# Performance work log

Hardware: AMD Instinct MI355X
Metric: run time of the kernel (lower is better)

## Reference

```python
import jax, jax.numpy as jnp
import numpy as np

D_MODEL = 512
N_HEADS = 8
MAX_DEPTH = 4
D_FF = 4 * D_MODEL
B, L = 4, 2048


def setup_inputs() -> dict:
    key = jax.random.key(0)
    ks = jax.random.split(key, 16)
    s = 0.02
    inp = {
        "x": jax.random.normal(ks[0], (B, L, D_MODEL), dtype=jnp.float32),
        # attention pre-norm
        "ln1_g": jnp.ones((D_MODEL,), jnp.float32),
        "ln1_b": jnp.zeros((D_MODEL,), jnp.float32),
        # MultiheadAttention in_proj (3D, D) and out_proj (D, D), torch (out, in) layout
        "Wqkv": jax.random.normal(ks[1], (3 * D_MODEL, D_MODEL), jnp.float32) * s,
        "bqkv": jnp.zeros((3 * D_MODEL,), jnp.float32),
        "Wo": jax.random.normal(ks[2], (D_MODEL, D_MODEL), jnp.float32) * s,
        "bo": jnp.zeros((D_MODEL,), jnp.float32),
        # FFN pre-norm + MLP
        "ln2_g": jnp.ones((D_MODEL,), jnp.float32),
        "ln2_b": jnp.zeros((D_MODEL,), jnp.float32),
        "W1": jax.random.normal(ks[3], (D_FF, D_MODEL), jnp.float32) * s,
        "b1": jnp.zeros((D_FF,), jnp.float32),
        "W2": jax.random.normal(ks[4], (D_MODEL, D_FF), jnp.float32) * s,
        "b2": jnp.zeros((D_MODEL,), jnp.float32),
        # token-choice depth router: LayerNorm + Linear(D,D) + GELU + Linear(D,max_depth)
        "rn_g": jnp.ones((D_MODEL,), jnp.float32),
        "rn_b": jnp.zeros((D_MODEL,), jnp.float32),
        "Rw1": jax.random.normal(ks[5], (D_MODEL, D_MODEL), jnp.float32) * s,
        "Rb1": jnp.zeros((D_MODEL,), jnp.float32),
        "Rw2": jax.random.normal(ks[6], (MAX_DEPTH, D_MODEL), jnp.float32) * s,
        "Rb2": jnp.zeros((MAX_DEPTH,), jnp.float32),
    }
    return inp


def _layernorm(x, g, b, eps=1e-5):
    mu = jnp.mean(x, axis=-1, keepdims=True)
    var = jnp.var(x, axis=-1, keepdims=True)
    return (x - mu) * jax.lax.rsqrt(var + eps) * g + b


def _block(x, ln1_g, ln1_b, Wqkv, bqkv, Wo, bo, ln2_g, ln2_b, W1, b1, W2, b2):
    Bb, Ll, D = x.shape
    H = N_HEADS
    dh = D // H
    # pre-norm self-attention
    h = _layernorm(x, ln1_g, ln1_b)
    qkv = h @ Wqkv.T + bqkv                      # (B, L, 3D)
    q, k, v = jnp.split(qkv, 3, axis=-1)
    q = q.reshape(Bb, Ll, H, dh)
    k = k.reshape(Bb, Ll, H, dh)
    v = v.reshape(Bb, Ll, H, dh)
    scores = jnp.einsum("blhd,bmhd->bhlm", q, k) / jnp.sqrt(jnp.float32(dh))
    attn = jax.nn.softmax(scores, axis=-1)
    o = jnp.einsum("bhlm,bmhd->blhd", attn, v).reshape(Bb, Ll, D)
    x = x + (o @ Wo.T + bo)
    # pre-norm FFN (exact-erf GELU, matching torch nn.GELU default)
    h2 = _layernorm(x, ln2_g, ln2_b)
    f = jax.nn.gelu(h2 @ W1.T + b1, approximate=False) @ W2.T + b2
    return x + f


def reference(x, ln1_g, ln1_b, Wqkv, bqkv, Wo, bo, ln2_g, ln2_b, W1, b1, W2, b2,
              rn_g, rn_b, Rw1, Rb1, Rw2, Rb2):
    # --- token-choice depth router (eval mode: argmax) ---
    rh = _layernorm(x, rn_g, rn_b)
    rh = jax.nn.gelu(rh @ Rw1.T + Rb1, approximate=False)
    router_logits = rh @ Rw2.T + Rb2             # (B, L, MAX_DEPTH)
    depths = jnp.argmax(router_logits, axis=-1) + 1  # (B, L) in [1, MAX_DEPTH]
    # --- dense recursion with torch.where-style selection ---
    cur = x
    for level in range(1, MAX_DEPTH + 1):
        upd = _block(cur, ln1_g, ln1_b, Wqkv, bqkv, Wo, bo,
                     ln2_g, ln2_b, W1, b1, W2, b2)
        keep = (depths >= level)[..., None]      # (B, L, 1)
        cur = jnp.where(keep, upd, cur)
    return cur, depths, router_logits
```

## Files before the change

kernel.cpp:

```cpp
#include <hip/hip_runtime.h>

typedef unsigned short u16;
typedef __attribute__((ext_vector_type(8))) short short8;
typedef __attribute__((ext_vector_type(4))) short s16x4;
typedef __attribute__((ext_vector_type(4))) float floatx4;
typedef __attribute__((ext_vector_type(4))) unsigned short u16x4;

#define NTOK 8192
#define DMODEL 512
#define DFF 2048
#define LSEQ 2048
#define RMARGIN 1e-3f

__device__ __forceinline__ u16 f2bf(float f) {
    union { float f; unsigned u; } x; x.f = f;
    unsigned r = (x.u + 0x7fffu + ((x.u >> 16) & 1u)) >> 16;
    return (u16)r;
}
__device__ __forceinline__ float bf2f(u16 h) {
    union { unsigned u; float f; } x; x.u = ((unsigned)h) << 16;
    return x.f;
}

__device__ __forceinline__ float geluf(float x) {
    return 0.5f * x * (1.0f + erff(x * 0.70710678118654752f));
}

__device__ __forceinline__ void gload_lds16(const void* g, void* l) {
    __builtin_amdgcn_global_load_lds(
        (const __attribute__((address_space(1))) void*)g,
        (__attribute__((address_space(3))) void*)l,
        16, 0, 0);
}

__device__ __forceinline__ s16x4 pack_p(float p0, float p1, float p2, float p3) {
    union { float f; unsigned u; } a{p0}, b{p1}, c{p2}, d{p3};
    union { unsigned u[2]; s16x4 s; } r;
    r.u[0] = (a.u >> 16) | (b.u & 0xffff0000u);
    r.u[1] = (c.u >> 16) | (d.u & 0xffff0000u);
    return r.s;
}

__global__ __launch_bounds__(256) void cvt_w(const float* __restrict__ wq,
                                             const float* __restrict__ wo,
                                             const float* __restrict__ w1,
                                             const float* __restrict__ w2,
                                             u16* __restrict__ out) {
    int i = blockIdx.x * 256 + threadIdx.x;
    float v;
    if (i < 786432)       v = wq[i];
    else if (i < 1048576) v = wo[i - 786432];
    else if (i < 2097152) v = w1[i - 1048576];
    else                  v = w2[i - 2097152];
    out[i] = f2bf(v);
}

__global__ __launch_bounds__(256) void copy_f32(const float* __restrict__ a,
                                                float* __restrict__ b) {
    size_t i = ((size_t)blockIdx.x * 256 + threadIdx.x) * 4;
    *(floatx4*)&b[i] = *(const floatx4*)&a[i];
}

__global__ __launch_bounds__(256) void cvt_rw1(const float* __restrict__ Rw1,
                                               u16* __restrict__ out) {
    const int i = blockIdx.x * 256 + threadIdx.x;
    const int n = i >> 9, k = i & 511;
    const float v = Rw1[i];
    const u16 hi = f2bf(v);
    const u16 lo = f2bf(v - bf2f(hi));
    out[(size_t)n * 1536 + k] = hi;
    out[(size_t)n * 1536 + 512 + k] = hi;
    out[(size_t)n * 1536 + 1024 + k] = lo;
}

__global__ __launch_bounds__(256) void cvt_split(const float* __restrict__ x,
                                                 u16* __restrict__ out,
                                                 int* __restrict__ cnt) {
    if (blockIdx.x == 0 && threadIdx.x == 0) *cnt = 0;
    const int i = blockIdx.x * 256 + threadIdx.x;
    const int base = i * 4;
    const int row = base >> 9, k = base & 511;
    const floatx4 v = *(const floatx4*)&x[base];
    u16x4 h, l;
#pragma unroll
    for (int e = 0; e < 4; ++e) {
        h[e] = f2bf(v[e]);
        l[e] = f2bf(v[e] - bf2f(h[e]));
    }
    u16* o = out + (size_t)row * 1536;
    *(u16x4*)&o[k] = h;
    *(u16x4*)&o[512 + k] = l;
    *(u16x4*)&o[1024 + k] = h;
}

template<bool OUTF32>
__global__ __launch_bounds__(256)
void ln_k(const float* __restrict__ x, const float* __restrict__ g,
          const float* __restrict__ bb, void* __restrict__ outp) {
    const int row = blockIdx.x * 4 + (threadIdx.x >> 6);
    const int lane = threadIdx.x & 63;
    const float* xr = x + (size_t)row * DMODEL;
    const int c0 = lane * 4, c1 = c0 + 256;
    floatx4 a = *(const floatx4*)&xr[c0];
    floatx4 b = *(const floatx4*)&xr[c1];
    float s = 0.f, sq = 0.f;
#pragma unroll
    for (int e = 0; e < 4; ++e) { s += a[e]; sq += a[e] * a[e]; }
#pragma unroll
    for (int e = 0; e < 4; ++e) { s += b[e]; sq += b[e] * b[e]; }
#pragma unroll
    for (int m = 32; m >= 1; m >>= 1) {
        s += __shfl_xor(s, m);
        sq += __shfl_xor(sq, m);
    }
    const float mean = s * (1.f / 512.f);
    const float rstd = rsqrtf(sq * (1.f / 512.f) - mean * mean + 1e-5f);
    floatx4 g0 = *(const floatx4*)&g[c0];
    floatx4 g1 = *(const floatx4*)&g[c1];
    floatx4 b0 = *(const floatx4*)&bb[c0];
    floatx4 b1 = *(const floatx4*)&bb[c1];
    floatx4 y0, y1;
#pragma unroll
    for (int e = 0; e < 4; ++e) {
        y0[e] = (a[e] - mean) * rstd * g0[e] + b0[e];
        y1[e] = (b[e] - mean) * rstd * g1[e] + b1[e];
    }
    if (OUTF32) {
        float* o = (float*)outp + (size_t)row * DMODEL;
        *(floatx4*)&o[c0] = y0;
        *(floatx4*)&o[c1] = y1;
    } else {
        u16* o = (u16*)outp + (size_t)row * DMODEL;
        u16x4 p0, p1;
#pragma unroll
        for (int e = 0; e < 4; ++e) { p0[e] = f2bf(y0[e]); p1[e] = f2bf(y1[e]); }
        *(u16x4*)&o[c0] = p0;
        *(u16x4*)&o[c1] = p1;
    }
}

template<int EPI, int BN>
__global__ __launch_bounds__(256, 2)
void gemm_bt(const u16* __restrict__ A, const u16* __restrict__ Bw,
             const float* __restrict__ bias,
             u16* __restrict__ Cb, float* __restrict__ Cf,
             const float* __restrict__ res, const float* __restrict__ depth,
             u16* __restrict__ Cv,
             float aux, int N, int K) {
    constexpr int NJ = BN / 32;
    __shared__ __align__(16) u16 As[128 * 32];
    __shared__ __align__(16) u16 Bs[BN * 32];
    const int tid = threadIdx.x;
    const int lane = tid & 63;
    const int w = tid >> 6;
    const int wm = (w >> 1) * 64;
    const int wn = (w & 1) * (BN / 2);
    const int mBase = blockIdx.x * 128;
    const int nBase = blockIdx.y * BN;
    const int q4 = lane >> 4, rl = lane & 15;

    floatx4 acc[4][NJ];
#pragma unroll
    for (int i = 0; i < 4; ++i)
#pragma unroll
        for (int j = 0; j < NJ; ++j) acc[i][j] = (floatx4){0.f, 0.f, 0.f, 0.f};

    const int i0 = tid, i1 = tid + 256;
    const int ar0 = i0 >> 2, ac0 = ((i0 & 3) ^ ((i0 >> 3) & 3)) * 8;
    const int ar1 = i1 >> 2, ac1 = ((i1 & 3) ^ ((i1 >> 3) & 3)) * 8;
    const u16* pA0 = A + (size_t)(mBase + ar0) * K + ac0;
    const u16* pA1 = A + (size_t)(mBase + ar1) * K + ac1;
    const u16* pB0 = Bw + (size_t)(nBase + ar0) * K + ac0;
    const u16* pB1 = (BN == 128) ? Bw + (size_t)(nBase + ar1) * K + ac1 : pB0;
    u16* lA0 = &As[i0 * 8];
    u16* lA1 = &As[i1 * 8];
    u16* lB0 = &Bs[i0 * 8];
    u16* lB1 = (BN == 128) ? &Bs[i1 * 8] : lB0;

    for (int k0 = 0; k0 < K; k0 += 32) {
        gload_lds16(pA0, lA0);
        gload_lds16(pA1, lA1);
        gload_lds16(pB0, lB0);
        if (BN == 128) gload_lds16(pB1, lB1);
        pA0 += 32; pA1 += 32; pB0 += 32;
        if (BN == 128) pB1 += 32;
        __syncthreads();
        short8 af[4], bf[NJ];
#pragma unroll
        for (int t = 0; t < 4; ++t) {
            const int r = wm + t * 16 + rl;
            af[t] = *(const short8*)&As[r * 32 + (q4 ^ ((r >> 1) & 3)) * 8];
        }
#pragma unroll
        for (int t = 0; t < NJ; ++t) {
            const int r = wn + t * 16 + rl;
            bf[t] = *(const short8*)&Bs[r * 32 + (q4 ^ ((r >> 1) & 3)) * 8];
        }
#pragma unroll
        for (int ti = 0; ti < 4; ++ti)
#pragma unroll
            for (int tj = 0; tj < NJ; ++tj)
                acc[ti][tj] = __builtin_amdgcn_mfma_f32_16x16x32_bf16(
                    af[ti], bf[tj], acc[ti][tj], 0, 0, 0);
        __syncthreads();
    }

#pragma unroll
    for (int ti = 0; ti < 4; ++ti) {
        const int r0 = mBase + wm + ti * 16 + q4 * 4;
#pragma unroll
        for (int tj = 0; tj < NJ; ++tj) {
            const int c = nBase + wn + tj * 16 + rl;
            const float bv = bias[c];
            if (EPI == 0) {
                if (nBase < 1024) {
                    const float sc = (nBase < 512) ? aux : 1.0f;
#pragma unroll
                    for (int rr = 0; rr < 4; ++rr)
                        Cb[(size_t)(r0 + rr) * 1024 + c] =
                            f2bf((acc[ti][tj][rr] + bv) * sc);
                } else {
                    const int cm = c - 1024;
                    const int hh = cm >> 6, dh = cm & 63;
                    const int bb2 = r0 >> 11, kv = r0 & 2047;
                    u16x4 pk;
#pragma unroll
                    for (int rr = 0; rr < 4; ++rr)
                        pk[rr] = f2bf(acc[ti][tj][rr] + bv);
                    *(u16x4*)&Cv[((size_t)(bb2 * 8 + hh) * 64 + dh) * 2048 + kv] = pk;
                }
            } else {
#pragma unroll
                for (int rr = 0; rr < 4; ++rr) {
                    const int r = r0 + rr;
                    const float v = acc[ti][tj][rr] + bv;
                    if (EPI == 1) {
                        Cb[(size_t)r * N + c] = f2bf(geluf(v));
                    } else if (EPI == 2) {
                        Cf[(size_t)r * N + c] = res[(size_t)r * N + c] + v;
                    } else if (EPI == 3) {
                        if (depth[r] >= aux)
                            Cf[(size_t)r * N + c] = res[(size_t)r * N + c] + v;
                    } else {
                        Cf[(size_t)r * N + c] = geluf(v);
                    }
                }
            }
        }
    }
}

__global__ __launch_bounds__(256, 2)
void attn_k(const u16* __restrict__ qk, const u16* __restrict__ vT,
            u16* __restrict__ o) {
    const int qt = blockIdx.x;
    const int bh = blockIdx.y;
    const int b = bh >> 3, h = bh & 7;
    const int tid = threadIdx.x, lane = tid & 63, w = tid >> 6;
    const int tok0 = b * LSEQ;
    const int qrow0 = qt * 128 + w * 32;
    const int q4 = lane >> 4, rl = lane & 15;

    __shared__ __align__(16) u16 Kt[128 * 64];
    __shared__ __align__(16) u16 Vt[64 * 128];

    const u16* vbase = vT + (size_t)bh * 64 * 2048;

    short8 qf[2][2];
#pragma unroll
    for (int nt = 0; nt < 2; ++nt)
#pragma unroll
        for (int ks = 0; ks < 2; ++ks)
            qf[nt][ks] = *(const short8*)&qk[(size_t)(tok0 + qrow0 + nt * 16 + rl) * 1024
                                             + h * 64 + ks * 32 + q4 * 8];

    floatx4 oacc[4][2];
#pragma unroll
    for (int dt = 0; dt < 4; ++dt)
#pragma unroll
        for (int nt = 0; nt < 2; ++nt) oacc[dt][nt] = (floatx4){0.f, 0.f, 0.f, 0.f};
    float lsum[2] = {0.f, 0.f};

    const u16* kp0 = &Kt[rl * 64 + ((q4 ^ (rl & 7))) * 8];
    const u16* kp1 = &Kt[rl * 64 + (((4 + q4) ^ (rl & 7))) * 8];

    for (int kt = 0; kt < 16; ++kt) {
        const int kv0 = kt * 128;
        __syncthreads();
#pragma unroll
        for (int it = 0; it < 4; ++it) {
            const int i = it * 256 + tid;
            const int r = i >> 3;
            const int c = ((i & 7) ^ (r & 7)) * 8;
            gload_lds16(&qk[(size_t)(tok0 + kv0 + r) * 1024 + 512 + h * 64 + c],
                        &Kt[i * 8]);
        }
#pragma unroll
        for (int it = 0; it < 4; ++it) {
            const int i = it * 256 + tid;
            const int dh = i >> 4;
            const int ch = (i & 15) ^ (dh & 15);
            gload_lds16(&vbase[(size_t)dh * 2048 + kv0 + ch * 8], &Vt[i * 8]);
        }
        __syncthreads();

#pragma unroll
        for (int mt = 0; mt < 8; ++mt) {
            const short8 kf0 = *(const short8*)&kp0[mt * 1024];
            const short8 kf1 = *(const short8*)&kp1[mt * 1024];
            floatx4 s[2];
#pragma unroll
            for (int nt = 0; nt < 2; ++nt) {
                s[nt] = __builtin_amdgcn_mfma_f32_16x16x32_bf16(kf0, qf[nt][0],
                        (floatx4){0.f, 0.f, 0.f, 0.f}, 0, 0, 0);
                s[nt] = __builtin_amdgcn_mfma_f32_16x16x32_bf16(kf1, qf[nt][1],
                        s[nt], 0, 0, 0);
            }
            s16x4 pb[2];
#pragma unroll
            for (int nt = 0; nt < 2; ++nt) {
                const float p0 = exp2f(s[nt][0]);
                const float p1 = exp2f(s[nt][1]);
                const float p2 = exp2f(s[nt][2]);
                const float p3 = exp2f(s[nt][3]);
                lsum[nt] += (p0 + p1) + (p2 + p3);
                pb[nt] = pack_p(p0, p1, p2, p3);
            }
            const int ct = 2 * mt + (q4 >> 1);
            const u16* vp = &Vt[(ct ^ rl) * 8 + (q4 & 1) * 4 + rl * 128];
#pragma unroll
            for (int dt = 0; dt < 4; ++dt) {
                const s16x4 vf = *(const s16x4*)&vp[dt * 2048];
#pragma unroll
                for (int nt = 0; nt < 2; ++nt)
                    oacc[dt][nt] = __builtin_amdgcn_mfma_f32_16x16x16bf16_1k(
                        vf, pb[nt], oacc[dt][nt], 0, 0, 0);
            }
        }
    }

#pragma unroll
    for (int nt = 0; nt < 2; ++nt) {
        float l = lsum[nt];
        l += __shfl_xor(l, 16);
        l += __shfl_xor(l, 32);
        const float inv = 1.0f / l;
        const size_t row = tok0 + qrow0 + nt * 16 + rl;
#pragma unroll
        for (int dt = 0; dt < 4; ++dt) {
            u16x4 pk;
#pragma unroll
            for (int rr = 0; rr < 4; ++rr) pk[rr] = f2bf(oacc[dt][nt][rr] * inv);
            *(u16x4*)&o[row * DMODEL + h * 64 + dt * 16 + q4 * 4] = pk;
        }
    }
}

__global__ __launch_bounds__(256)
void router_logits_f32(const float* __restrict__ rr, const float* __restrict__ Rw2,
                       const float* __restrict__ Rb2, float* __restrict__ logits,
                       float* __restrict__ depthf, int* __restrict__ cnt,
                       int* __restrict__ list) {
    const int t = blockIdx.x * 4 + (threadIdx.x >> 6);
    const int lane = threadIdx.x & 63;
    const float* xr = rr + (size_t)t * 512;
    const int c0 = lane * 4, c1 = c0 + 256;
    floatx4 a = *(const floatx4*)&xr[c0];
    floatx4 b = *(const floatx4*)&xr[c1];
    float s[4];
#pragma unroll
    for (int d = 0; d < 4; ++d) {
        const float* wr = Rw2 + d * 512;
        floatx4 wa = *(const floatx4*)&wr[c0];
        floatx4 wb = *(const floatx4*)&wr[c1];
        float acc = 0.f;
#pragma unroll
        for (int e = 0; e < 4; ++e) acc += a[e] * wa[e];
#pragma unroll
        for (int e = 0; e < 4; ++e) acc += b[e] * wb[e];
        s[d] = acc;
    }
#pragma unroll
    for (int m = 32; m >= 1; m >>= 1)
#pragma unroll
        for (int d = 0; d < 4; ++d) s[d] += __shfl_xor(s[d], m);
    if (lane == 0) {
        float v[4];
        float bv = -1e30f; int best = 0;
#pragma unroll
        for (int d = 0; d < 4; ++d) {
            v[d] = s[d] + Rb2[d];
            logits[(size_t)t * 4 + d] = v[d];
            if (v[d] > bv) { bv = v[d]; best = d; }
        }
        float second = -1e30f;
#pragma unroll
        for (int d = 0; d < 4; ++d)
            if (d != best) second = fmaxf(second, v[d]);
        depthf[t] = (float)(best + 1);
        if (bv - second < RMARGIN) {
            int idx = atomicAdd(cnt, 1);
            list[idx] = t;
        }
    }
}

__global__ __launch_bounds__(256)
void router_exact(const float* __restrict__ rh, const float* __restrict__ Rw1,
                  const float* __restrict__ Rb1, const float* __restrict__ Rw2,
                  const float* __restrict__ Rb2, const int* __restrict__ cnt,
                  const int* __restrict__ list, float* __restrict__ logits,
                  float* __restrict__ depthf) {
    __shared__ float rhs[512];
    __shared__ double rrd[512];
    __shared__ double lg[4];
    const int n = *cnt;
    const int tid = threadIdx.x;
    for (int ii = blockIdx.x; ii < n; ii += gridDim.x) {
        const int t = list[ii];
        rhs[tid] = rh[(size_t)t * 512 + tid];
        rhs[tid + 256] = rh[(size_t)t * 512 + 256 + tid];
        __syncthreads();
#pragma unroll
        for (int oo = 0; oo < 2; ++oo) {
            const int nn = tid + oo * 256;
            double acc = (double)Rb1[nn];
            const float* wrow = Rw1 + (size_t)nn * 512;
            for (int k = 0; k < 512; ++k)
                acc = fma((double)rhs[k], (double)wrow[k], acc);
            rrd[nn] = 0.5 * acc * (1.0 + erf(acc * 0.70710678118654752440));
        }
        __syncthreads();
        const int w = tid >> 6, lane = tid & 63;
        double acc2 = 0.0;
        for (int k = lane; k < 512; k += 64)
            acc2 += rrd[k] * (double)Rw2[w * 512 + k];
#pragma unroll
        for (int m = 32; m >= 1; m >>= 1) acc2 += __shfl_xor(acc2, m);
        if (lane == 0) lg[w] = acc2 + (double)Rb2[w];
        __syncthreads();
        if (tid == 0) {
            double bv = -1e300; int best = 0;
#pragma unroll
            for (int d = 0; d < 4; ++d) {
                const double v = lg[d];
                logits[(size_t)t * 4 + d] = (float)v;
                if (v > bv) { bv = v; best = d; }
            }
            depthf[t] = (float)(best + 1);
        }
        __syncthreads();
    }
}

extern "C" void kernel_launch(void* const* d_in, const int* in_sizes, int n_in,
                              void* d_out, int out_size, void* d_ws, size_t ws_size,
                              hipStream_t stream) {
    (void)in_sizes; (void)n_in; (void)out_size; (void)ws_size;
    const float* x    = (const float*)d_in[0];
    const float* ln1g = (const float*)d_in[1];
    const float* ln1b = (const float*)d_in[2];
    const float* Wqkv = (const float*)d_in[3];
    const float* bqkv = (const float*)d_in[4];
    const float* Wo   = (const float*)d_in[5];
    const float* bo   = (const float*)d_in[6];
    const float* ln2g = (const float*)d_in[7];
    const float* ln2b = (const float*)d_in[8];
    const float* W1   = (const float*)d_in[9];
    const float* b1   = (const float*)d_in[10];
    const float* W2   = (const float*)d_in[11];
    const float* b2   = (const float*)d_in[12];
    const float* rng  = (const float*)d_in[13];
    const float* rnb  = (const float*)d_in[14];
    const float* Rw1  = (const float*)d_in[15];
    const float* Rb1  = (const float*)d_in[16];
    const float* Rw2  = (const float*)d_in[17];
    const float* Rb2  = (const float*)d_in[18];

    float* cur    = (float*)d_out;
    float* depthf = cur + (size_t)NTOK * DMODEL;
    float* logits = depthf + NTOK;

    char* ws = (char*)d_ws;
    float* xmid = (float*)ws;
    u16* sbuf   = (u16*)(ws + 16777216);
    u16* qk     = (u16*)(ws + 25165824);
    u16* ffb    = (u16*)(ws + 41943040);
    u16* vTb    = (u16*)(ws + 75497472);
    u16* wbf    = (u16*)(ws + 83886080);

    u16* rw1s   = (u16*)(ws + 16777216);
    int* rcnt   = (int*)(ws + 18874368);
    int* rlist  = rcnt + 16;
    u16* asplit = ffb;
    float* rrf  = (float*)qk;

    u16* wq = wbf;
    u16* wo = wbf + 786432;
    u16* w1 = wbf + 1048576;
    u16* w2 = wbf + 2097152;

    const float qsc = 0.125f * 1.4426950408889634f;

    cvt_w<<<12288, 256, 0, stream>>>(Wqkv, Wo, W1, W2, wbf);
    copy_f32<<<4096, 256, 0, stream>>>(x, cur);

    ln_k<true><<<2048, 256, 0, stream>>>(x, rng, rnb, xmid);
    cvt_rw1<<<1024, 256, 0, stream>>>(Rw1, rw1s);
    cvt_split<<<4096, 256, 0, stream>>>(xmid, asplit, rcnt);
    gemm_bt<4, 64><<<dim3(64, 8), 256, 0, stream>>>(
        asplit, rw1s, Rb1, nullptr, rrf, nullptr, nullptr, nullptr, 0.f, 512, 1536);
    router_logits_f32<<<2048, 256, 0, stream>>>(rrf, Rw2, Rb2, logits, depthf,
                                                rcnt, rlist);
    router_exact<<<128, 256, 0, stream>>>(xmid, Rw1, Rb1, Rw2, Rb2, rcnt, rlist,
                                          logits, depthf);

    for (int level = 1; level <= 4; ++level) {
        ln_k<false><<<2048, 256, 0, stream>>>(cur, ln1g, ln1b, sbuf);
        gemm_bt<0, 128><<<dim3(64, 12), 256, 0, stream>>>(
            sbuf, wq, bqkv, qk, nullptr, nullptr, nullptr, vTb, qsc, 1536, 512);
        attn_k<<<dim3(16, 32), 256, 0, stream>>>(qk, vTb, sbuf);
        gemm_bt<2, 64><<<dim3(64, 8), 256, 0, stream>>>(
            sbuf, wo, bo, nullptr, xmid, cur, nullptr, nullptr, 0.f, 512, 512);
        ln_k<false><<<2048, 256, 0, stream>>>(xmid, ln2g, ln2b, sbuf);
        gemm_bt<1, 128><<<dim3(64, 16), 256, 0, stream>>>(
            sbuf, w1, b1, ffb, nullptr, nullptr, nullptr, nullptr, 0.f, 2048, 512);
        gemm_bt<3, 64><<<dim3(64, 8), 256, 0, stream>>>(
            ffb, w2, b2, nullptr, cur, xmid, depthf, nullptr, (float)level, 512, 2048);
    }
}
```

Before: 913.8 us.

## Compact active tokens per level and skip work for tokens past their depth

Adds a build_idx kernel that builds a per-batch compacted list of token indices whose routed depth reaches each level. Attention queries, the output projection, the second layernorm and both FFN GEMMs now run only on compacted rows, and whole blocks past the active count exit early. Results are scattered back to the original token positions in the final residual epilogue. Keys and values are still computed for all tokens, so attention stays exact. This adds an atomic-based index build and gather/scatter indexing in the epilogues, and the row order within a level depends on atomic ordering.

Result: slower. 1.089 ms (+19.1%).

```diff
diff --git a/kernel.cpp b/kernel.cpp
--- a/kernel.cpp
+++ b/kernel.cpp
@@ -75,8 +75,11 @@
 
 __global__ __launch_bounds__(256) void cvt_split(const float* __restrict__ x,
                                                  u16* __restrict__ out,
-                                                 int* __restrict__ cnt) {
+                                                 int* __restrict__ cnt,
+                                                 int* __restrict__ bcnt) {
     if (blockIdx.x == 0 && threadIdx.x == 0) *cnt = 0;
+    if (blockIdx.x == 0 && threadIdx.x < 16)
+        bcnt[threadIdx.x] = (threadIdx.x < 4) ? 2048 : 0;
     const int i = blockIdx.x * 256 + threadIdx.x;
     const int base = i * 4;
     const int row = base >> 9, k = base & 511;
@@ -93,11 +96,31 @@
     *(u16x4*)&o[1024 + k] = h;
 }
 
-template<bool OUTF32>
+__global__ __launch_bounds__(256)
+void build_idx(const float* __restrict__ depthf, int* __restrict__ bcnt,
+               int* __restrict__ idx) {
+    const int t = blockIdx.x * 256 + threadIdx.x;
+    const int b = t >> 11;
+    const int d = (int)depthf[t];
+    idx[t] = t;
+#pragma unroll
+    for (int lvl = 2; lvl <= 4; ++lvl) {
+        if (d >= lvl) {
+            const int p = atomicAdd(&bcnt[(lvl - 1) * 4 + b], 1);
+            idx[(lvl - 1) * 8192 + (b << 11) + p] = t;
+        }
+    }
+}
+
+template<bool OUTF32, bool GATED>
 __global__ __launch_bounds__(256)
 void ln_k(const float* __restrict__ x, const float* __restrict__ g,
-          const float* __restrict__ bb, void* __restrict__ outp) {
+          const float* __restrict__ bb, void* __restrict__ outp,
+          const int* __restrict__ bcnt) {
     const int row = blockIdx.x * 4 + (threadIdx.x >> 6);
+    if (GATED) {
+        if ((row & 2047) >= bcnt[row >> 11]) return;
+    }
     const int lane = threadIdx.x & 63;
     const float* xr = x + (size_t)row * DMODEL;
     const int c0 = lane * 4, c1 = c0 + 256;
@@ -144,10 +167,18 @@
 void gemm_bt(const u16* __restrict__ A, const u16* __restrict__ Bw,
              const float* __restrict__ bias,
              u16* __restrict__ Cb, float* __restrict__ Cf,
-             const float* __restrict__ res, const float* __restrict__ depth,
+             const float* __restrict__ res,
+             const int* __restrict__ IDX, const int* __restrict__ bcnt,
              u16* __restrict__ Cv,
              float aux, int N, int K) {
     constexpr int NJ = BN / 32;
+    constexpr bool GATED = (EPI == 1 || EPI == 2 || EPI == 3);
+    const int mBase = blockIdx.x * 128;
+    int cntb = 0;
+    if (GATED) {
+        cntb = bcnt[mBase >> 11];
+        if ((mBase & 2047) >= cntb) return;
+    }
     __shared__ __align__(16) u16 As[128 * 32];
     __shared__ __align__(16) u16 Bs[BN * 32];
     const int tid = threadIdx.x;
@@ -155,7 +186,6 @@
     const int w = tid >> 6;
     const int wm = (w >> 1) * 64;
     const int wn = (w & 1) * (BN / 2);
-    const int mBase = blockIdx.x * 128;
     const int nBase = blockIdx.y * BN;
     const int q4 = lane >> 4, rl = lane & 15;
 
@@ -208,6 +238,12 @@
 #pragma unroll
     for (int ti = 0; ti < 4; ++ti) {
         const int r0 = mBase + wm + ti * 16 + q4 * 4;
+        int toks[4];
+        if (EPI == 2 || EPI == 3) {
+#pragma unroll
+            for (int rr = 0; rr < 4; ++rr)
+                toks[rr] = ((r0 + rr) & 2047) < cntb ? IDX[r0 + rr] : -1;
+        }
 #pragma unroll
         for (int tj = 0; tj < NJ; ++tj) {
             const int c = nBase + wn + tj * 16 + rl;
@@ -237,10 +273,13 @@
                     if (EPI == 1) {
                         Cb[(size_t)r * N + c] = f2bf(geluf(v));
                     } else if (EPI == 2) {
-                        Cf[(size_t)r * N + c] = res[(size_t)r * N + c] + v;
+                        if (toks[rr] >= 0)
+                            Cf[(size_t)r * N + c] =
+                                res[(size_t)toks[rr] * N + c] + v;
                     } else if (EPI == 3) {
-                        if (depth[r] >= aux)
-                            Cf[(size_t)r * N + c] = res[(size_t)r * N + c] + v;
+                        if (toks[rr] >= 0)
+                            Cf[(size_t)toks[rr] * N + c] =
+                                res[(size_t)r * N + c] + v;
                     } else {
                         Cf[(size_t)r * N + c] = geluf(v);
                     }
@@ -252,13 +291,16 @@
 
 __global__ __launch_bounds__(256, 2)
 void attn_k(const u16* __restrict__ qk, const u16* __restrict__ vT,
-            u16* __restrict__ o) {
+            u16* __restrict__ o, const int* __restrict__ IDX,
+            const int* __restrict__ bcnt) {
     const int qt = blockIdx.x;
     const int bh = blockIdx.y;
     const int b = bh >> 3, h = bh & 7;
+    const int cnt = bcnt[b];
+    if (qt * 128 >= cnt) return;
     const int tid = threadIdx.x, lane = tid & 63, w = tid >> 6;
     const int tok0 = b * LSEQ;
-    const int qrow0 = qt * 128 + w * 32;
+    const int seg = b << 11;
     const int q4 = lane >> 4, rl = lane & 15;
 
     __shared__ __align__(16) u16 Kt[128 * 64];
@@ -266,13 +308,17 @@
 
     const u16* vbase = vT + (size_t)bh * 64 * 2048;
 
+    const int pos0 = qt * 128 + w * 32 + rl;
+    const int pos1 = pos0 + 16;
+    const int tA = (pos0 < cnt) ? IDX[seg + pos0] : tok0;
+    const int tB = (pos1 < cnt) ? IDX[seg + pos1] : tok0;
+
     short8 qf[2][2];
 #pragma unroll
-    for (int nt = 0; nt < 2; ++nt)
-#pragma unroll
-        for (int ks = 0; ks < 2; ++ks)
-            qf[nt][ks] = *(const short8*)&qk[(size_t)(tok0 + qrow0 + nt * 16 + rl) * 1024
-                                             + h * 64 + ks * 32 + q4 * 8];
+    for (int ks = 0; ks < 2; ++ks) {
+        qf[0][ks] = *(const short8*)&qk[(size_t)tA * 1024 + h * 64 + ks * 32 + q4 * 8];
+        qf[1][ks] = *(const short8*)&qk[(size_t)tB * 1024 + h * 64 + ks * 32 + q4 * 8];
+    }
 
     floatx4 oacc[4][2];
 #pragma unroll
@@ -345,13 +391,16 @@
         l += __shfl_xor(l, 16);
         l += __shfl_xor(l, 32);
         const float inv = 1.0f / l;
-        const size_t row = tok0 + qrow0 + nt * 16 + rl;
-#pragma unroll
-        for (int dt = 0; dt < 4; ++dt) {
-            u16x4 pk;
-#pragma unroll
-            for (int rr = 0; rr < 4; ++rr) pk[rr] = f2bf(oacc[dt][nt][rr] * inv);
-            *(u16x4*)&o[row * DMODEL + h * 64 + dt * 16 + q4 * 4] = pk;
+        const int pos = (nt == 0) ? pos0 : pos1;
+        if (pos < cnt) {
+            const size_t row = seg + pos;
+#pragma unroll
+            for (int dt = 0; dt < 4; ++dt) {
+                u16x4 pk;
+#pragma unroll
+                for (int rr = 0; rr < 4; ++rr) pk[rr] = f2bf(oacc[dt][nt][rr] * inv);
+                *(u16x4*)&o[row * DMODEL + h * 64 + dt * 16 + q4 * 4] = pk;
+            }
         }
     }
 }
@@ -488,6 +537,8 @@
     u16* ffb    = (u16*)(ws + 41943040);
     u16* vTb    = (u16*)(ws + 75497472);
     u16* wbf    = (u16*)(ws + 83886080);
+    int* idxb   = (int*)(ws + 90177536);
+    int* bcntb  = (int*)(ws + 90308608);
 
     u16* rw1s   = (u16*)(ws + 16777216);
     int* rcnt   = (int*)(ws + 18874368);
@@ -505,27 +556,34 @@
     cvt_w<<<12288, 256, 0, stream>>>(Wqkv, Wo, W1, W2, wbf);
     copy_f32<<<4096, 256, 0, stream>>>(x, cur);
 
-    ln_k<true><<<2048, 256, 0, stream>>>(x, rng, rnb, xmid);
+    ln_k<true, false><<<2048, 256, 0, stream>>>(x, rng, rnb, xmid, nullptr);
     cvt_rw1<<<1024, 256, 0, stream>>>(Rw1, rw1s);
-    cvt_split<<<4096, 256, 0, stream>>>(xmid, asplit, rcnt);
+    cvt_split<<<4096, 256, 0, stream>>>(xmid, asplit, rcnt, bcntb);
     gemm_bt<4, 64><<<dim3(64, 8), 256, 0, stream>>>(
-        asplit, rw1s, Rb1, nullptr, rrf, nullptr, nullptr, nullptr, 0.f, 512, 1536);
+        asplit, rw1s, Rb1, nullptr, rrf, nullptr, nullptr, nullptr, nullptr,
+        0.f, 512, 1536);
     router_logits_f32<<<2048, 256, 0, stream>>>(rrf, Rw2, Rb2, logits, depthf,
                                                 rcnt, rlist);
     router_exact<<<128, 256, 0, stream>>>(xmid, Rw1, Rb1, Rw2, Rb2, rcnt, rlist,
                                           logits, depthf);
+    build_idx<<<32, 256, 0, stream>>>(depthf, bcntb, idxb);
 
     for (int level = 1; level <= 4; ++level) {
-        ln_k<false><<<2048, 256, 0, stream>>>(cur, ln1g, ln1b, sbuf);
+        const int* IDXl = idxb + (level - 1) * 8192;
+        const int* bcl  = bcntb + (level - 1) * 4;
+        ln_k<false, false><<<2048, 256, 0, stream>>>(cur, ln1g, ln1b, sbuf, nullptr);
         gemm_bt<0, 128><<<dim3(64, 12), 256, 0, stream>>>(
-            sbuf, wq, bqkv, qk, nullptr, nullptr, nullptr, vTb, qsc, 1536, 512);
-        attn_k<<<dim3(16, 32), 256, 0, stream>>>(qk, vTb, sbuf);
+            sbuf, wq, bqkv, qk, nullptr, nullptr, nullptr, nullptr, vTb,
+            qsc, 1536, 512);
+        attn_k<<<dim3(16, 32), 256, 0, stream>>>(qk, vTb, sbuf, IDXl, bcl);
         gemm_bt<2, 64><<<dim3(64, 8), 256, 0, stream>>>(
-            sbuf, wo, bo, nullptr, xmid, cur, nullptr, nullptr, 0.f, 512, 512);
-        ln_k<false><<<2048, 256, 0, stream>>>(xmid, ln2g, ln2b, sbuf);
+            sbuf, wo, bo, nullptr, xmid, cur, IDXl, bcl, nullptr, 0.f, 512, 512);
+        ln_k<false, true><<<2048, 256, 0, stream>>>(xmid, ln2g, ln2b, sbuf, bcl);
         gemm_bt<1, 128><<<dim3(64, 16), 256, 0, stream>>>(
-            sbuf, w1, b1, ffb, nullptr, nullptr, nullptr, nullptr, 0.f, 2048, 512);
+            sbuf, w1, b1, ffb, nullptr, nullptr, nullptr, bcl, nullptr,
+            0.f, 2048, 512);
         gemm_bt<3, 64><<<dim3(64, 8), 256, 0, stream>>>(
-            ffb, w2, b2, nullptr, cur, xmid, depthf, nullptr, (float)level, 512, 2048);
-    }
-}
+            ffb, w2, b2, nullptr, cur, xmid, IDXl, bcl, nullptr,
+            0.f, 512, 2048);
+    }
+}
```
